# Kernel tuning notes

Measured on AMD Instinct MI355X. Metric: run time of the kernel, lower is better.

Reference implementation:

```python
import jax, jax.numpy as jnp
from jax import lax
import numpy as np

K = 31      # avg_pool2d kernel_size
PAD = 15    # avg_pool2d padding
EPS = 1.0
GAMMA = 5.0


def _box_avg(x):
    # Separable 31x31 box filter, stride 1, zero padding 15,
    # count_include_pad=True (PyTorch default) -> always divide by K*K.
    s = lax.reduce_window(x, 0.0, lax.add, (1, 1, K, 1), (1, 1, 1, 1),
                          [(0, 0), (0, 0), (PAD, PAD), (0, 0)])
    s = lax.reduce_window(s, 0.0, lax.add, (1, 1, 1, K), (1, 1, 1, 1),
                          [(0, 0), (0, 0), (0, 0), (PAD, PAD)])
    return s / (K * K)


def setup_inputs() -> dict:
    key = jax.random.key(0)
    k1, k2 = jax.random.split(key)
    shape = (64, 1, 512, 512)  # [B, C, H, W]
    inp = jax.random.uniform(k1, shape, dtype=jnp.float32)
    tgt = jax.random.uniform(k2, shape, dtype=jnp.float32)
    return {"input": inp, "target": tgt}


def reference(input, target):
    weight = 1.0 + GAMMA * jnp.abs(_box_avg(target) - target)
    intersection = jnp.sum(input * target * weight)
    denom = jnp.sum(input * weight) + jnp.sum(target * weight)
    dice = (2.0 * intersection + EPS) / (denom + EPS)
    return 1.0 - dice
```

## Files before the change

### kernel.cpp

```cpp
#include <hip/hip_runtime.h>


#define BATCH 64
#define H     512
#define W     512
#define PADR  15
#define RBAND 64
#define RING  38
#define NBLK  (BATCH * (H / RBAND))

__global__ __launch_bounds__(256) void fused_kernel(const float* __restrict__ tgt,
                                                    const float* __restrict__ inp,
                                                    float4* __restrict__ partials) {
    const int tid  = threadIdx.x;
    const int lane = tid & 63;
    const int wv   = tid >> 6;
    const int blk  = blockIdx.x;
    const int band = blk & 7;
    const int b    = blk >> 3;
    const int R0   = band * RBAND;
    const float* timg = tgt + (size_t)b * H * W;
    const float* iimg = inp + (size_t)b * H * W;

    __shared__ __align__(16) float ring[RING * W];

    #pragma unroll
    for (int it = 0; it < 19; ++it) {
        const int u     = tid + it * 256;
        const int r_off = u >> 7;
        const int c4    = (u & 127) * 4;
        const int row   = R0 - 15 + r_off;
        float4 v = make_float4(0.f, 0.f, 0.f, 0.f);
        if (row >= 0 && row < H) v = *(const float4*)(timg + (size_t)row * W + c4);
        *(float4*)&ring[((row + RING) % RING) * W + c4] = v;
    }
    __syncthreads();

    const float mL1 = (lane >= 1) ? 1.f : 0.f;
    const float mR1 = (lane <= 62) ? 1.f : 0.f;
    const float mL2 = (lane >= 2) ? 1.f : 0.f;
    const float mR2 = (lane <= 61) ? 1.f : 0.f;
    const int col0 = lane * 8;

    float vr[8];
    #pragma unroll
    for (int k = 0; k < 8; ++k) vr[k] = 0.f;
    #pragma unroll
    for (int jj = -PADR; jj <= PADR; ++jj) {
        const int rr = R0 + wv + jj;
        const int sl = ((rr + RING) % RING) * W + col0;
        const float4 a = *(const float4*)&ring[sl];
        const float4 c = *(const float4*)&ring[sl + 4];
        vr[0] += a.x; vr[1] += a.y; vr[2] += a.z; vr[3] += a.w;
        vr[4] += c.x; vr[5] += c.y; vr[6] += c.z; vr[7] += c.w;
    }

    const float inv = 1.0f / 961.0f;
    float aI = 0.f, aA = 0.f, aB = 0.f;

    for (int j = 0; j < 16; ++j) {
        const int h = R0 + 4 * j + wv;

        float4 pf0 = make_float4(0.f, 0.f, 0.f, 0.f), pf1 = pf0;
        const int prow = R0 + 4 * j + 23 + wv;
        if (j < 14 && prow < H) {
            pf0 = *(const float4*)(timg + (size_t)prow * W + col0);
            pf1 = *(const float4*)(timg + (size_t)prow * W + col0 + 4);
        }
        const float4 i0 = *(const float4*)(iimg + (size_t)h * W + col0);
        const float4 i1 = *(const float4*)(iimg + (size_t)h * W + col0 + 4);

        const float p1 = vr[0];
        const float p2 = p1 + vr[1];
        const float p3 = p2 + vr[2];
        const float p4 = p3 + vr[3];
        const float p5 = p4 + vr[4];
        const float p6 = p5 + vr[5];
        const float p7 = p6 + vr[6];
        const float s  = p7 + vr[7];
        const float f1 = s - p1, f2 = s - p2, f3 = s - p3, f4 = s - p4;
        const float f5 = s - p5, f6 = s - p6, f7 = s - p7;

        const float sL1 = __shfl_up(s, 1, 64);
        const float sR1 = __shfl_down(s, 1, 64);
        const float g1 = __shfl_up(f1, 2, 64);
        const float g2 = __shfl_up(f2, 2, 64);
        const float g3 = __shfl_up(f3, 2, 64);
        const float g4 = __shfl_up(f4, 2, 64);
        const float g5 = __shfl_up(f5, 2, 64);
        const float g6 = __shfl_up(f6, 2, 64);
        const float g7 = __shfl_up(f7, 2, 64);
        const float q1 = __shfl_down(p1, 2, 64);
        const float q2 = __shfl_down(p2, 2, 64);
        const float q3 = __shfl_down(p3, 2, 64);
        const float q4 = __shfl_down(p4, 2, 64);
        const float q5 = __shfl_down(p5, 2, 64);
        const float q6 = __shfl_down(p6, 2, 64);
        const float q7 = __shfl_down(p7, 2, 64);

        const float S3 = fmaf(mL1, sL1, fmaf(mR1, sR1, s));
        float win[8];
        win[0] = fmaf(mL2, g1, S3);
        win[1] = fmaf(mL2, g2, fmaf(mR2, q1, S3));
        win[2] = fmaf(mL2, g3, fmaf(mR2, q2, S3));
        win[3] = fmaf(mL2, g4, fmaf(mR2, q3, S3));
        win[4] = fmaf(mL2, g5, fmaf(mR2, q4, S3));
        win[5] = fmaf(mL2, g6, fmaf(mR2, q5, S3));
        win[6] = fmaf(mL2, g7, fmaf(mR2, q6, S3));
        win[7] = fmaf(mR2, q7, S3);

        const int slC = (h % RING) * W + col0;
        const float4 t0 = *(const float4*)&ring[slC];
        const float4 t1 = *(const float4*)&ring[slC + 4];
        const float tv[8] = {t0.x, t0.y, t0.z, t0.w, t1.x, t1.y, t1.z, t1.w};
        const float iv[8] = {i0.x, i0.y, i0.z, i0.w, i1.x, i1.y, i1.z, i1.w};

        #pragma unroll
        for (int k = 0; k < 8; ++k) {
            const float wgt = fmaf(5.0f, fabsf(fmaf(win[k], inv, -tv[k])), 1.0f);
            aI += iv[k] * tv[k] * wgt;
            aA += iv[k] * wgt;
            aB += tv[k] * wgt;
        }

        if (j < 15) {
            #pragma unroll
            for (int q = 0; q < 4; ++q) {
                const int slA = ((h + 16 + q) % RING) * W + col0;
                const int slS = (((h - 15 + q) + RING) % RING) * W + col0;
                const float4 a0 = *(const float4*)&ring[slA];
                const float4 a1 = *(const float4*)&ring[slA + 4];
                const float4 s0 = *(const float4*)&ring[slS];
                const float4 s1 = *(const float4*)&ring[slS + 4];
                vr[0] += a0.x - s0.x; vr[1] += a0.y - s0.y;
                vr[2] += a0.z - s0.z; vr[3] += a0.w - s0.w;
                vr[4] += a1.x - s1.x; vr[5] += a1.y - s1.y;
                vr[6] += a1.z - s1.z; vr[7] += a1.w - s1.w;
            }
        }
        __syncthreads();

        if (j < 14) {
            const int sl = (prow % RING) * W + col0;
            *(float4*)&ring[sl]     = pf0;
            *(float4*)&ring[sl + 4] = pf1;
        }
        __syncthreads();
    }

    #pragma unroll
    for (int off = 32; off > 0; off >>= 1) {
        aI += __shfl_down(aI, off, 64);
        aA += __shfl_down(aA, off, 64);
        aB += __shfl_down(aB, off, 64);
    }
    if (lane == 0) { ring[wv] = aI; ring[8 + wv] = aA; ring[16 + wv] = aB; }
    __syncthreads();
    if (tid == 0) {
        float4 o;
        o.x = ring[0] + ring[1] + ring[2] + ring[3];
        o.y = ring[8] + ring[9] + ring[10] + ring[11];
        o.z = ring[16] + ring[17] + ring[18] + ring[19];
        o.w = 0.f;
        partials[blk] = o;
    }
}

__global__ __launch_bounds__(512) void reduce_kernel(const float4* __restrict__ partials,
                                                     float* __restrict__ out) {
    const int tid = threadIdx.x;
    const float4 v = partials[tid];
    float aI = v.x, aA = v.y, aB = v.z;
    #pragma unroll
    for (int off = 32; off > 0; off >>= 1) {
        aI += __shfl_down(aI, off, 64);
        aA += __shfl_down(aA, off, 64);
        aB += __shfl_down(aB, off, 64);
    }
    __shared__ float s[3][8];
    const int wvx = tid >> 6, ln = tid & 63;
    if (ln == 0) { s[0][wvx] = aI; s[1][wvx] = aA; s[2][wvx] = aB; }
    __syncthreads();
    if (tid == 0) {
        float I = 0.f, A = 0.f, Bv = 0.f;
        #pragma unroll
        for (int k = 0; k < 8; ++k) { I += s[0][k]; A += s[1][k]; Bv += s[2][k]; }
        out[0] = 1.0f - (2.0f * I + 1.0f) / (A + Bv + 1.0f);
    }
}

extern "C" void kernel_launch(void* const* d_in, const int* in_sizes, int n_in,
                              void* d_out, int out_size, void* d_ws, size_t ws_size,
                              hipStream_t stream) {
    const float* inp = (const float*)d_in[0];
    const float* tgt = (const float*)d_in[1];
    float* out = (float*)d_out;

    float4* partials = (float4*)d_ws;

    fused_kernel<<<NBLK, 256, 0, stream>>>(tgt, inp, partials);
    reduce_kernel<<<1, 512, 0, stream>>>(partials, out);
}
```

Before: 152.0 us.

## Interleave ring row layout to avoid LDS bank conflicts and hoist ring loads

Each ring row is now stored as two halves: a lane's first float4 goes at lane*4 and its second at 256+lane*4. This replaces the earlier contiguous 8-float-per-lane layout, which had an 8-float stride between lanes' float4 accesses and caused LDS bank conflicts. The initial fill is rewritten so each wave loads whole rows in the same per-lane pattern. The centre-row and sliding-window ring reads are also moved ahead of the horizontal shuffle math, so LDS latency can overlap compute. The cost is higher register pressure from holding 16 float4 values live.

```diff
diff --git a/kernel.cpp b/kernel.cpp
--- a/kernel.cpp
+++ b/kernel.cpp
@@ -24,15 +24,23 @@
 
     __shared__ __align__(16) float ring[RING * W];
 
-    #pragma unroll
-    for (int it = 0; it < 19; ++it) {
-        const int u     = tid + it * 256;
-        const int r_off = u >> 7;
-        const int c4    = (u & 127) * 4;
-        const int row   = R0 - 15 + r_off;
-        float4 v = make_float4(0.f, 0.f, 0.f, 0.f);
-        if (row >= 0 && row < H) v = *(const float4*)(timg + (size_t)row * W + c4);
-        *(float4*)&ring[((row + RING) % RING) * W + c4] = v;
+    const int col0 = lane * 8;
+    const int ofsE = lane * 4;
+    const int ofsO = 256 + lane * 4;
+
+    for (int k = 0; k < 10; ++k) {
+        const int r_off = wv + 4 * k;
+        if (r_off < RING) {
+            const int row = R0 - 15 + r_off;
+            float4 v0 = make_float4(0.f, 0.f, 0.f, 0.f), v1 = v0;
+            if (row >= 0 && row < H) {
+                v0 = *(const float4*)(timg + (size_t)row * W + col0);
+                v1 = *(const float4*)(timg + (size_t)row * W + col0 + 4);
+            }
+            const int slot = (row + RING) % RING;
+            *(float4*)&ring[slot * W + ofsE] = v0;
+            *(float4*)&ring[slot * W + ofsO] = v1;
+        }
     }
     __syncthreads();
 
@@ -40,7 +48,6 @@
     const float mR1 = (lane <= 62) ? 1.f : 0.f;
     const float mL2 = (lane >= 2) ? 1.f : 0.f;
     const float mR2 = (lane <= 61) ? 1.f : 0.f;
-    const int col0 = lane * 8;
 
     float vr[8];
     #pragma unroll
@@ -48,9 +55,9 @@
     #pragma unroll
     for (int jj = -PADR; jj <= PADR; ++jj) {
         const int rr = R0 + wv + jj;
-        const int sl = ((rr + RING) % RING) * W + col0;
-        const float4 a = *(const float4*)&ring[sl];
-        const float4 c = *(const float4*)&ring[sl + 4];
+        const int sl = ((rr + RING) % RING) * W;
+        const float4 a = *(const float4*)&ring[sl + ofsE];
+        const float4 c = *(const float4*)&ring[sl + ofsO];
         vr[0] += a.x; vr[1] += a.y; vr[2] += a.z; vr[3] += a.w;
         vr[4] += c.x; vr[5] += c.y; vr[6] += c.z; vr[7] += c.w;
     }
@@ -69,6 +76,23 @@
         }
         const float4 i0 = *(const float4*)(iimg + (size_t)h * W + col0);
         const float4 i1 = *(const float4*)(iimg + (size_t)h * W + col0 + 4);
+
+        const int slC = (h % RING) * W;
+        const float4 t0 = *(const float4*)&ring[slC + ofsE];
+        const float4 t1 = *(const float4*)&ring[slC + ofsO];
+
+        float4 adv0[4], adv1[4], sb0[4], sb1[4];
+        if (j < 15) {
+            #pragma unroll
+            for (int q = 0; q < 4; ++q) {
+                const int slA = ((h + 16 + q) % RING) * W;
+                const int slS = (((h - 15 + q) + RING) % RING) * W;
+                adv0[q] = *(const float4*)&ring[slA + ofsE];
+                adv1[q] = *(const float4*)&ring[slA + ofsO];
+                sb0[q]  = *(const float4*)&ring[slS + ofsE];
+                sb1[q]  = *(const float4*)&ring[slS + ofsO];
+            }
+        }
 
         const float p1 = vr[0];
         const float p2 = p1 + vr[1];
@@ -109,9 +133,6 @@
         win[6] = fmaf(mL2, g7, fmaf(mR2, q6, S3));
         win[7] = fmaf(mR2, q7, S3);
 
-        const int slC = (h % RING) * W + col0;
-        const float4 t0 = *(const float4*)&ring[slC];
-        const float4 t1 = *(const float4*)&ring[slC + 4];
         const float tv[8] = {t0.x, t0.y, t0.z, t0.w, t1.x, t1.y, t1.z, t1.w};
         const float iv[8] = {i0.x, i0.y, i0.z, i0.w, i1.x, i1.y, i1.z, i1.w};
 
@@ -126,24 +147,18 @@
         if (j < 15) {
             #pragma unroll
             for (int q = 0; q < 4; ++q) {
-                const int slA = ((h + 16 + q) % RING) * W + col0;
-                const int slS = (((h - 15 + q) + RING) % RING) * W + col0;
-                const float4 a0 = *(const float4*)&ring[slA];
-                const float4 a1 = *(const float4*)&ring[slA + 4];
-                const float4 s0 = *(const float4*)&ring[slS];
-                const float4 s1 = *(const float4*)&ring[slS + 4];
-                vr[0] += a0.x - s0.x; vr[1] += a0.y - s0.y;
-                vr[2] += a0.z - s0.z; vr[3] += a0.w - s0.w;
-                vr[4] += a1.x - s1.x; vr[5] += a1.y - s1.y;
-                vr[6] += a1.z - s1.z; vr[7] += a1.w - s1.w;
+                vr[0] += adv0[q].x - sb0[q].x; vr[1] += adv0[q].y - sb0[q].y;
+                vr[2] += adv0[q].z - sb0[q].z; vr[3] += adv0[q].w - sb0[q].w;
+                vr[4] += adv1[q].x - sb1[q].x; vr[5] += adv1[q].y - sb1[q].y;
+                vr[6] += adv1[q].z - sb1[q].z; vr[7] += adv1[q].w - sb1[q].w;
             }
         }
         __syncthreads();
 
         if (j < 14) {
-            const int sl = (prow % RING) * W + col0;
-            *(float4*)&ring[sl]     = pf0;
-            *(float4*)&ring[sl + 4] = pf1;
+            const int sl = (prow % RING) * W;
+            *(float4*)&ring[sl + ofsE] = pf0;
+            *(float4*)&ring[sl + ofsO] = pf1;
         }
         __syncthreads();
     }
```

Result: no change. 150.2 us (-1.2%).
